# Kernel optimization log

Measured on AMD Instinct MI355X. Metric: run time of the kernel, lower is better.

The kernel has to match this reference:

```python
import jax, jax.numpy as jnp
import numpy as np

NUM_REL = 3


def _inter_layer(h_tail_all, self_tail, self_full, adj, idx, alpha):
    """One InterAgg layer (vectorized over 3 relations' IntraAgg + softmax fusion).
    h_tail_all: [N, d]  last-d features of previous layer for ALL nodes
    self_tail:  [n, d]  same features for the batch nodes
    self_full:  [n, D]  full previous-layer features for the batch nodes
    adj:        [3, N, K] neighbor indices
    idx:        [n]      batch node indices
    alpha:      [2d, 3]  relation attention params
    returns [n, D + 2d]
    """
    W = jax.nn.softmax(alpha, axis=1)  # [2d, 3]
    weighted = jnp.zeros((idx.shape[0], alpha.shape[0]), dtype=h_tail_all.dtype)
    for r in range(NUM_REL):  # fixed small structural loop
        neigh = adj[r][idx]                       # [n, K]
        mean = h_tail_all[neigh].mean(axis=1)     # [n, d]  neighbor-mean (IntraAgg _feats_1)
        intra = jnp.concatenate([mean, self_tail - mean], axis=1)  # [n, 2d]
        weighted = weighted + intra * W[:, r]     # softmax-weighted relation fusion
    return jnp.concatenate([self_full, weighted], axis=1)


def setup_inputs() -> dict:
    key = jax.random.key(0)
    ks = jax.random.split(key, 8)
    N, K, d, B = 50000, 32, 64, 1024
    return {
        "feat_data": jax.random.normal(ks[0], (N, 25), dtype=jnp.float32),
        "W_mlp": jax.random.normal(ks[1], (25, d), dtype=jnp.float32) * 0.2,
        "alpha1": jax.random.normal(ks[2], (2 * d, 3), dtype=jnp.float32) * 0.1,
        "alpha2": jax.random.normal(ks[3], (4 * d, 3), dtype=jnp.float32) * 0.1,
        "linear_w": jax.random.normal(ks[4], (7 * d, 2), dtype=jnp.float32) * 0.05,
        "prior": jax.random.uniform(ks[5], (2,), dtype=jnp.float32, minval=0.01, maxval=1.0),
        "adj": jax.random.randint(ks[6], (3, N, K), 0, N, dtype=jnp.int32),
        "nodes": jax.random.randint(ks[7], (B,), 0, N, dtype=jnp.int32),
    }


def reference(feat_data, W_mlp, alpha1, alpha2, linear_w, prior, adj, nodes):
    N = feat_data.shape[0]
    d = W_mlp.shape[1]
    # MLP layer (layer 0): per-node linear projection
    h0 = feat_data @ W_mlp                                   # [N, d]
    # InterAgg layer 1 over all nodes (so layer 2 can gather neighbor features)
    all_idx = jnp.arange(N)
    h1 = _inter_layer(h0, h0, h0, adj, all_idx, alpha1)      # [N, 3d]
    # InterAgg layer 2 over the batch nodes; uses last 2d cols of layer-1 output
    self_full = h1[nodes]                                    # [B, 3d]
    self_tail = self_full[:, -2 * d:]                        # [B, 2d]
    h2 = _inter_layer(h1[:, -2 * d:], self_tail, self_full, adj, nodes, alpha2)  # [B, 7d]
    # Final linear + log-prior
    return h2 @ linear_w + jnp.log(prior)                    # [B, 2]
```

## Files before the change

### kernel.cpp

```cpp
#include <hip/hip_runtime.h>

typedef unsigned int u32;
typedef unsigned short u16;
typedef _Float16 f16;
typedef __attribute__((ext_vector_type(2))) _Float16 f16x2;
typedef __attribute__((ext_vector_type(4))) _Float16 f16x4;
typedef __attribute__((ext_vector_type(8))) _Float16 f16x8;
typedef __attribute__((ext_vector_type(4))) float f32x4;

#if __has_builtin(__builtin_amdgcn_mfma_f32_16x16x16f16)
#define USE_K16 1
#else
#define USE_K16 0
#endif

__device__ __forceinline__ float bf16_lo(u32 u) { u32 x = u << 16; return __builtin_bit_cast(float, x); }
__device__ __forceinline__ float bf16_hi(u32 u) { u32 x = u & 0xffff0000u; return __builtin_bit_cast(float, x); }
__device__ __forceinline__ float bf16f(u16 v) { u32 x = ((u32)v) << 16; return __builtin_bit_cast(float, x); }
__device__ __forceinline__ u16 f2bf(float f) {
    u32 x = __builtin_bit_cast(u32, f);
    return (u16)((x + 0x7fffu + ((x >> 16) & 1u)) >> 16);
}

__global__ __launch_bounds__(256) void k_prep(const float* __restrict__ feat,
                                              u16* __restrict__ featp, int N) {
    int t = blockIdx.x * 256 + threadIdx.x;
    int row = t >> 5, col = t & 31;
    if (row >= N) return;
    featp[(size_t)row * 32 + col] = (col < 25) ? f2bf(feat[(size_t)row * 25 + col]) : (u16)0;
}

__device__ float m_val(int row, int col, const float* __restrict__ W,
                       const float* __restrict__ a1) {
    if (row >= 84) {
        int k = row - 84;
        return (k < 25 && col >= 64) ? W[k * 64 + (col - 64)] : 0.f;
    }
    int seg = (row >= 56) ? 2 : (row >= 28) ? 1 : 0;
    int k = row - seg * 28;
    if (k >= 25) return 0.f;
    int cc = (col < 64) ? col : col - 64;
    int arow = (col < 64) ? cc : 64 + cc;
    float e0 = __expf(a1[arow * 3 + 0]);
    float e1 = __expf(a1[arow * 3 + 1]);
    float e2 = __expf(a1[arow * 3 + 2]);
    float wt = ((seg == 0) ? e0 : (seg == 1) ? e1 : e2) / (e0 + e1 + e2);
    float v = W[k * 64 + cc] * wt * (1.f / 32.f);
    return (col < 64) ? v : -v;
}

__global__ __launch_bounds__(256) void k_prepM(const float* __restrict__ W,
                                               const float* __restrict__ a1,
                                               f16* __restrict__ Bpack) {
    int idx = blockIdx.x * 256 + threadIdx.x;
#if USE_K16
    int j = idx & 3, l = (idx >> 2) & 63, ks = (idx >> 8) & 7, ct = idx >> 11;
    int row = ks * 16 + ((l >> 4) << 2) + j;
#else
    int j = idx & 7, l = (idx >> 3) & 63, ks = (idx >> 9) & 3, ct = idx >> 11;
    int row = ks * 32 + ((l >> 4) << 3) + j;
#endif
    int col = ct * 16 + (l & 15);
    float v = (row < 112) ? m_val(row, col, W, a1) : 0.f;
    Bpack[idx] = (f16)v;
}

__global__ __launch_bounds__(256) void k_gather(const float* __restrict__ feat,
                                                const u16* __restrict__ featp,
                                                const int* __restrict__ adj,
                                                f16* __restrict__ xbuf, int N) {
    int wave = threadIdx.x >> 6;
    int lane = threadIdx.x & 63;
    int i = blockIdx.x * 4 + wave;
    if (i >= N) return;
    int g = lane >> 4;
    int c = lane & 15;

    const u32* fp = (const u32*)featp;

#pragma unroll
    for (int r = 0; r < 3; ++r) {
        const int* arow = adj + ((size_t)r * N + i) * 32;
        float s0 = 0.f, s1 = 0.f;
#pragma unroll
        for (int it = 0; it < 8; ++it) {
            int nb = arow[it * 4 + g];
            u32 u = fp[nb * 16 + c];
            s0 += bf16_lo(u);
            s1 += bf16_hi(u);
        }
        s0 += __shfl_xor(s0, 16, 64); s0 += __shfl_xor(s0, 32, 64);
        s1 += __shfl_xor(s1, 16, 64); s1 += __shfl_xor(s1, 32, 64);
        if (g == 0 && c < 14) {
            f16x2 o;
            o[0] = (f16)s0;
            o[1] = (f16)s1;
            *(u32*)(xbuf + (size_t)i * 128 + r * 28 + 2 * c) = __builtin_bit_cast(u32, o);
        }
    }
    if (lane < 28)
        xbuf[(size_t)i * 128 + 84 + lane] = (lane < 25) ? (f16)feat[(size_t)i * 25 + lane] : (f16)0.f;
}

__global__ __launch_bounds__(256) void k_mfma(const f16* __restrict__ xbuf,
                                              const f16* __restrict__ Bpack,
                                              u16* __restrict__ w1, int N) {
    int unit = blockIdx.x * 4 + (threadIdx.x >> 6);
    if (unit * 16 >= N) return;
    int l = threadIdx.x & 63;
    int i0 = unit * 16;
#if USE_K16
    f16x4 a[8];
    const f16* xrow = xbuf + (size_t)(i0 + (l & 15)) * 128 + ((l >> 4) << 2);
#pragma unroll
    for (int ks = 0; ks < 8; ++ks) a[ks] = *(const f16x4*)(xrow + ks * 16);
#pragma unroll
    for (int ct = 0; ct < 8; ++ct) {
        f32x4 d = {0.f, 0.f, 0.f, 0.f};
        const f16* bp = Bpack + ((size_t)(ct * 8) * 64 + l) * 4;
#pragma unroll
        for (int ks = 0; ks < 8; ++ks) {
            f16x4 b = *(const f16x4*)(bp + ks * 256);
            d = __builtin_amdgcn_mfma_f32_16x16x16f16(a[ks], b, d, 0, 0, 0);
        }
#pragma unroll
        for (int reg = 0; reg < 4; ++reg) {
            int node = i0 + ((l >> 4) << 2) + reg;
            if (node < N) w1[(size_t)node * 128 + ct * 16 + (l & 15)] = f2bf(d[reg]);
        }
    }
#else
    f16x8 a[4];
    const f16* xrow = xbuf + (size_t)(i0 + (l & 15)) * 128 + ((l >> 4) << 3);
#pragma unroll
    for (int ks = 0; ks < 4; ++ks) a[ks] = *(const f16x8*)(xrow + ks * 32);
#pragma unroll
    for (int ct = 0; ct < 8; ++ct) {
        f32x4 d = {0.f, 0.f, 0.f, 0.f};
        const f16* bp = Bpack + ((size_t)(ct * 4) * 64 + l) * 8;
#pragma unroll
        for (int ks = 0; ks < 4; ++ks) {
            f16x8 b = *(const f16x8*)(bp + ks * 512);
            d = __builtin_amdgcn_mfma_f32_16x16x32_f16(a[ks], b, d, 0, 0, 0);
        }
#pragma unroll
        for (int reg = 0; reg < 4; ++reg) {
            int node = i0 + ((l >> 4) << 2) + reg;
            if (node < N) w1[(size_t)node * 128 + ct * 16 + (l & 15)] = f2bf(d[reg]);
        }
    }
#endif
}

__global__ __launch_bounds__(128) void k_layer2(const float* __restrict__ feat,
                                                const float* __restrict__ Wmlp,
                                                const u16* __restrict__ w1h,
                                                const float* __restrict__ alpha2,
                                                const float* __restrict__ lw,
                                                const float* __restrict__ prior,
                                                const int* __restrict__ adj,
                                                const int* __restrict__ nodes,
                                                float* __restrict__ out, int N) {
    __shared__ int s_idx[96];
    __shared__ float s_red[4];
    int b = blockIdx.x;
    int i = nodes[b];
    int t = threadIdx.x;

    if (t < 96) {
        int r = t >> 5, k = t & 31;
        s_idx[t] = adj[((size_t)r * N + i) * 32 + k];
    }
    __syncthreads();

    float mean[3];
#pragma unroll
    for (int r = 0; r < 3; ++r) {
        float acc = 0.f;
#pragma unroll
        for (int k = 0; k < 32; ++k)
            acc += bf16f(w1h[(size_t)s_idx[r * 32 + k] * 128 + t]);
        mean[r] = acc * (1.f / 32.f);
    }

    float et[3], eb[3], st = 0.f, sb = 0.f;
#pragma unroll
    for (int r = 0; r < 3; ++r) {
        et[r] = __expf(alpha2[t * 3 + r]);         st += et[r];
        eb[r] = __expf(alpha2[(128 + t) * 3 + r]); sb += eb[r];
    }
    float t2 = 0.f, wb = 0.f;
#pragma unroll
    for (int r = 0; r < 3; ++r) { t2 += et[r] * mean[r]; wb += eb[r] * mean[r]; }
    t2 /= st;
    wb /= sb;

    float t1 = bf16f(w1h[(size_t)i * 128 + t]);
    float t3 = t1 - wb;

    float p0 = t1 * lw[(64 + t) * 2 + 0] + t2 * lw[(192 + t) * 2 + 0] + t3 * lw[(320 + t) * 2 + 0];
    float p1 = t1 * lw[(64 + t) * 2 + 1] + t2 * lw[(192 + t) * 2 + 1] + t3 * lw[(320 + t) * 2 + 1];
    if (t < 64) {
        float t0 = 0.f;
#pragma unroll
        for (int k = 0; k < 25; ++k) t0 += feat[(size_t)i * 25 + k] * Wmlp[k * 64 + t];
        p0 += t0 * lw[t * 2 + 0];
        p1 += t0 * lw[t * 2 + 1];
    }

#pragma unroll
    for (int off = 32; off > 0; off >>= 1) {
        p0 += __shfl_down(p0, off, 64);
        p1 += __shfl_down(p1, off, 64);
    }
    int wv = t >> 6, lane = t & 63;
    if (lane == 0) { s_red[wv * 2 + 0] = p0; s_red[wv * 2 + 1] = p1; }
    __syncthreads();
    if (t == 0) {
        out[b * 2 + 0] = s_red[0] + s_red[2] + __logf(prior[0]);
        out[b * 2 + 1] = s_red[1] + s_red[3] + __logf(prior[1]);
    }
}

extern "C" void kernel_launch(void* const* d_in, const int* in_sizes, int n_in,
                              void* d_out, int out_size, void* d_ws, size_t ws_size,
                              hipStream_t stream) {
    const float* feat   = (const float*)d_in[0];
    const float* Wmlp   = (const float*)d_in[1];
    const float* alpha1 = (const float*)d_in[2];
    const float* alpha2 = (const float*)d_in[3];
    const float* lw     = (const float*)d_in[4];
    const float* prior  = (const float*)d_in[5];
    const int*   adj    = (const int*)d_in[6];
    const int*   nodes  = (const int*)d_in[7];
    float* out = (float*)d_out;

    int N = in_sizes[0] / 25;
    int B = in_sizes[7];

    char* base = (char*)d_ws;
    u16* featp = (u16*)base;
    u16* w1    = (u16*)base;
    f16* xbuf  = (f16*)(base + (size_t)N * 128 * 2);
    f16* Bpack = (f16*)(base + (size_t)N * 128 * 2 + (size_t)N * 128 * 2);

    k_prep  <<<(N * 32 + 255) / 256, 256, 0, stream>>>(feat, featp, N);
    k_prepM <<<64,                   256, 0, stream>>>(Wmlp, alpha1, Bpack);
    k_gather<<<(N + 3) / 4,          256, 0, stream>>>(feat, featp, adj, xbuf, N);
    k_mfma  <<<((N + 15) / 16 + 3) / 4, 256, 0, stream>>>(xbuf, Bpack, w1, N);
    k_layer2<<<B,                    128, 0, stream>>>(feat, Wmlp, w1, alpha2, lw, prior, adj, nodes, out, N);
}
```

Baseline: 66.42 us.

## Fuse layer-1 neighbor gather with MFMA projection via shared-memory staging

Merges the gather kernel and the MFMA kernel into one kernel. Each block gathers neighbor sums for 16 nodes into an LDS tile, then each wave computes two column tiles with MFMA. The xbuf round trip through global memory and one launch go away. The gather is reorganized so each 16-lane group handles one node, broadcasting adjacency indices with shuffles instead of the cross-group reduction. The workspace is re-laid out so w1 no longer aliases featp. Risks are lower parallelism per node during the gather and a block-level sync.

```diff
diff --git a/kernel.cpp b/kernel.cpp
--- a/kernel.cpp
+++ b/kernel.cpp
@@ -65,57 +65,64 @@
     Bpack[idx] = (f16)v;
 }
 
-__global__ __launch_bounds__(256) void k_gather(const float* __restrict__ feat,
-                                                const u16* __restrict__ featp,
-                                                const int* __restrict__ adj,
-                                                f16* __restrict__ xbuf, int N) {
-    int wave = threadIdx.x >> 6;
-    int lane = threadIdx.x & 63;
-    int i = blockIdx.x * 4 + wave;
-    if (i >= N) return;
-    int g = lane >> 4;
-    int c = lane & 15;
+__global__ __launch_bounds__(256) void k_layer1f(const float* __restrict__ feat,
+                                                 const u16* __restrict__ featp,
+                                                 const int* __restrict__ adj,
+                                                 const f16* __restrict__ Bpack,
+                                                 u16* __restrict__ w1, int N) {
+    __shared__ f16 x[16][136];
+    int w = threadIdx.x >> 6;
+    int l = threadIdx.x & 63;
+    int g = l >> 4;
+    int c = l & 15;
+    int i0 = blockIdx.x * 16;
+    int node = i0 + w * 4 + g;
+    int nsafe = (node < N) ? node : 0;
 
     const u32* fp = (const u32*)featp;
-
 #pragma unroll
     for (int r = 0; r < 3; ++r) {
-        const int* arow = adj + ((size_t)r * N + i) * 32;
+        const int* arow = adj + ((size_t)r * N + nsafe) * 32;
+        int idxA = __builtin_nontemporal_load(arow + c);
+        int idxB = __builtin_nontemporal_load(arow + 16 + c);
         float s0 = 0.f, s1 = 0.f;
 #pragma unroll
-        for (int it = 0; it < 8; ++it) {
-            int nb = arow[it * 4 + g];
-            u32 u = fp[nb * 16 + c];
+        for (int k = 0; k < 16; ++k) {
+            int nb = __shfl(idxA, k, 16);
+            u32 u = fp[(size_t)nb * 16 + c];
             s0 += bf16_lo(u);
             s1 += bf16_hi(u);
         }
-        s0 += __shfl_xor(s0, 16, 64); s0 += __shfl_xor(s0, 32, 64);
-        s1 += __shfl_xor(s1, 16, 64); s1 += __shfl_xor(s1, 32, 64);
-        if (g == 0 && c < 14) {
+#pragma unroll
+        for (int k = 0; k < 16; ++k) {
+            int nb = __shfl(idxB, k, 16);
+            u32 u = fp[(size_t)nb * 16 + c];
+            s0 += bf16_lo(u);
+            s1 += bf16_hi(u);
+        }
+        if (c < 14) {
             f16x2 o;
             o[0] = (f16)s0;
             o[1] = (f16)s1;
-            *(u32*)(xbuf + (size_t)i * 128 + r * 28 + 2 * c) = __builtin_bit_cast(u32, o);
-        }
-    }
-    if (lane < 28)
-        xbuf[(size_t)i * 128 + 84 + lane] = (lane < 25) ? (f16)feat[(size_t)i * 25 + lane] : (f16)0.f;
-}
-
-__global__ __launch_bounds__(256) void k_mfma(const f16* __restrict__ xbuf,
-                                              const f16* __restrict__ Bpack,
-                                              u16* __restrict__ w1, int N) {
-    int unit = blockIdx.x * 4 + (threadIdx.x >> 6);
-    if (unit * 16 >= N) return;
-    int l = threadIdx.x & 63;
-    int i0 = unit * 16;
+            *(u32*)&x[w * 4 + g][r * 28 + 2 * c] = __builtin_bit_cast(u32, o);
+        }
+    }
+    for (int e = threadIdx.x; e < 16 * 44; e += 256) {
+        int row = e / 44, col = 84 + e % 44;
+        int nrow = i0 + row;
+        float v = (col < 109 && nrow < N) ? feat[(size_t)nrow * 25 + (col - 84)] : 0.f;
+        x[row][col] = (f16)v;
+    }
+    __syncthreads();
+
 #if USE_K16
     f16x4 a[8];
-    const f16* xrow = xbuf + (size_t)(i0 + (l & 15)) * 128 + ((l >> 4) << 2);
+    const f16* xrow = &x[l & 15][(l >> 4) << 2];
 #pragma unroll
     for (int ks = 0; ks < 8; ++ks) a[ks] = *(const f16x4*)(xrow + ks * 16);
 #pragma unroll
-    for (int ct = 0; ct < 8; ++ct) {
+    for (int ctt = 0; ctt < 2; ++ctt) {
+        int ct = w * 2 + ctt;
         f32x4 d = {0.f, 0.f, 0.f, 0.f};
         const f16* bp = Bpack + ((size_t)(ct * 8) * 64 + l) * 4;
 #pragma unroll
@@ -125,17 +132,18 @@
         }
 #pragma unroll
         for (int reg = 0; reg < 4; ++reg) {
-            int node = i0 + ((l >> 4) << 2) + reg;
-            if (node < N) w1[(size_t)node * 128 + ct * 16 + (l & 15)] = f2bf(d[reg]);
+            int n2 = i0 + ((l >> 4) << 2) + reg;
+            if (n2 < N) w1[(size_t)n2 * 128 + ct * 16 + (l & 15)] = f2bf(d[reg]);
         }
     }
 #else
     f16x8 a[4];
-    const f16* xrow = xbuf + (size_t)(i0 + (l & 15)) * 128 + ((l >> 4) << 3);
+    const f16* xrow = &x[l & 15][(l >> 4) << 3];
 #pragma unroll
     for (int ks = 0; ks < 4; ++ks) a[ks] = *(const f16x8*)(xrow + ks * 32);
 #pragma unroll
-    for (int ct = 0; ct < 8; ++ct) {
+    for (int ctt = 0; ctt < 2; ++ctt) {
+        int ct = w * 2 + ctt;
         f32x4 d = {0.f, 0.f, 0.f, 0.f};
         const f16* bp = Bpack + ((size_t)(ct * 4) * 64 + l) * 8;
 #pragma unroll
@@ -145,8 +153,8 @@
         }
 #pragma unroll
         for (int reg = 0; reg < 4; ++reg) {
-            int node = i0 + ((l >> 4) << 2) + reg;
-            if (node < N) w1[(size_t)node * 128 + ct * 16 + (l & 15)] = f2bf(d[reg]);
+            int n2 = i0 + ((l >> 4) << 2) + reg;
+            if (n2 < N) w1[(size_t)n2 * 128 + ct * 16 + (l & 15)] = f2bf(d[reg]);
         }
     }
 #endif
@@ -240,13 +248,11 @@
 
     char* base = (char*)d_ws;
     u16* featp = (u16*)base;
-    u16* w1    = (u16*)base;
-    f16* xbuf  = (f16*)(base + (size_t)N * 128 * 2);
-    f16* Bpack = (f16*)(base + (size_t)N * 128 * 2 + (size_t)N * 128 * 2);
-
-    k_prep  <<<(N * 32 + 255) / 256, 256, 0, stream>>>(feat, featp, N);
-    k_prepM <<<64,                   256, 0, stream>>>(Wmlp, alpha1, Bpack);
-    k_gather<<<(N + 3) / 4,          256, 0, stream>>>(feat, featp, adj, xbuf, N);
-    k_mfma  <<<((N + 15) / 16 + 3) / 4, 256, 0, stream>>>(xbuf, Bpack, w1, N);
-    k_layer2<<<B,                    128, 0, stream>>>(feat, Wmlp, w1, alpha2, lw, prior, adj, nodes, out, N);
-}
+    u16* w1    = (u16*)(base + (size_t)N * 32 * 2);
+    f16* Bpack = (f16*)(base + (size_t)N * 32 * 2 + (size_t)N * 128 * 2);
+
+    k_prep   <<<(N * 32 + 255) / 256, 256, 0, stream>>>(feat, featp, N);
+    k_prepM  <<<64,                   256, 0, stream>>>(Wmlp, alpha1, Bpack);
+    k_layer1f<<<(N + 15) / 16,        256, 0, stream>>>(feat, featp, adj, Bpack, w1, N);
+    k_layer2 <<<B,                    128, 0, stream>>>(feat, Wmlp, w1, alpha2, lw, prior, adj, nodes, out, N);
+}
```

New measurement: 60.34 us. 9.2% less time.
